# Kernel tuning notes

Measured on AMD Instinct MI355X. Metric: run time of the kernel, lower is better.

The kernel has to match this reference:

```python
import jax, jax.numpy as jnp
import numpy as np

H = 128   # hidden_dim
L = 3     # num_layers
N = 50000
E = 800000
EPS = 1e-5


def setup_inputs() -> dict:
    key = jax.random.key(0)
    ks = jax.random.split(key, 16)
    s = 0.02  # param init scale
    return {
        "edge_index_new": jax.random.randint(ks[0], (2, E), 0, N),
        "aligned_features": jax.random.normal(ks[1], (E, 8), jnp.float32),
        "h_nodes_old": jax.random.normal(ks[2], (N, H), jnp.float32),
        "num_nodes": N,
        # node_fusion: Linear(2H -> H)
        "Wf": jax.random.normal(ks[3], (2 * H, H), jnp.float32) * s,
        "bf": jnp.zeros((H,), jnp.float32),
        # edge_to_weight: Linear(8->H), Linear(H->1)
        "We1": jax.random.normal(ks[4], (8, H), jnp.float32) * s,
        "be1": jnp.zeros((H,), jnp.float32),
        "We2": jax.random.normal(ks[5], (H, 1), jnp.float32) * s,
        "be2": jnp.zeros((1,), jnp.float32),
        # GraphConv per layer: lin_rel (W+b), lin_root (W, no bias)
        "Wrel": jax.random.normal(ks[6], (L, H, H), jnp.float32) * s,
        "brel": jnp.zeros((L, H), jnp.float32),
        "Wroot": jax.random.normal(ks[7], (L, H, H), jnp.float32) * s,
        # LayerNorm per layer
        "gamma": jnp.ones((L, H), jnp.float32),
        "beta": jnp.zeros((L, H), jnp.float32),
        # edge_decoder: Linear(2H+8 -> H), Linear(H -> 1)
        "Wd1": jax.random.normal(ks[8], (2 * H + 8, H), jnp.float32) * s,
        "bd1": jnp.zeros((H,), jnp.float32),
        "Wd2": jax.random.normal(ks[9], (H, 1), jnp.float32) * s,
        "bd2": jnp.zeros((1,), jnp.float32),
    }


def _layer_norm(x, g, b):
    mu = jnp.mean(x, axis=-1, keepdims=True)
    var = jnp.mean((x - mu) ** 2, axis=-1, keepdims=True)
    return (x - mu) * jax.lax.rsqrt(var + EPS) * g + b


def reference(edge_index_new, aligned_features, h_nodes_old, num_nodes,
              Wf, bf, We1, be1, We2, be2,
              Wrel, brel, Wroot, gamma, beta,
              Wd1, bd1, Wd2, bd2):
    dt = h_nodes_old.dtype
    hd = Wf.shape[1]
    # node_fusion(cat([ones, h_old])) ; dropout is identity in eval
    x_init = jnp.ones((num_nodes, hd), dtype=dt)
    x = jax.nn.relu(jnp.concatenate([x_init, h_nodes_old], axis=-1) @ Wf + bf)
    # edge_to_weight -> scalar per edge
    ew = jax.nn.sigmoid(jax.nn.relu(aligned_features @ We1 + be1) @ We2 + be2)[:, 0]
    src, dst = edge_index_new[0], edge_index_new[1]
    n_layers = Wrel.shape[0]
    for l in range(n_layers):
        x_res = x
        # GraphConv: sum_{j->i} w_e * x[j], then lin_rel(agg) + lin_root(x)
        msg = ew[:, None] * x[src]                         # [E, H]
        agg = jax.ops.segment_sum(msg, dst, num_segments=num_nodes)
        h = agg @ Wrel[l] + brel[l] + x @ Wroot[l]
        h = jax.nn.relu(_layer_norm(h, gamma[l], beta[l]))
        x = h + x_res
    # edge decoder on gathered node pairs + raw 8-dim features
    edge_repr = jnp.concatenate([x[src], x[dst], aligned_features], axis=-1)
    hmid = jax.nn.relu(edge_repr @ Wd1 + bd1)
    return hmid @ Wd2 + bd2
```

## Files before the change

### kernel.cpp

```cpp
#include <hip/hip_runtime.h>
#include <hip/hip_bf16.h>

#define H 128
#define LN_EPS 1e-5f

typedef __attribute__((ext_vector_type(8))) short bf16x8;
typedef __attribute__((ext_vector_type(4))) float f32x4;

static __device__ __forceinline__ unsigned short f2bf(float f) {
  unsigned u = __float_as_uint(f);
  unsigned r = (u + 0x7fff + ((u >> 16) & 1)) >> 16;
  return (unsigned short)r;
}
static __device__ __forceinline__ float bf2f(unsigned short s) {
  return __uint_as_float(((unsigned)s) << 16);
}


__global__ void zero_int_kernel(int* __restrict__ p, int n) {
  int i = blockIdx.x * blockDim.x + threadIdx.x;
  if (i < n) p[i] = 0;
}

__global__ __launch_bounds__(1024) void prep_cvec_kernel(const float* __restrict__ Wf,
                                                         const float* __restrict__ bf,
                                                         float* __restrict__ cvec) {
  __shared__ float part[8][128];
  int tid = threadIdx.x;
  int col = tid & 127, seg = tid >> 7;
  float s = 0.f;
  for (int r = seg * 16; r < seg * 16 + 16; ++r) s += Wf[r * H + col];
  part[seg][col] = s;
  __syncthreads();
  if (tid < 128) {
    float t = bf[tid];
#pragma unroll
    for (int g = 0; g < 8; ++g) t += part[g][tid];
    cvec[tid] = t;
  }
}

__global__ void count_kernel(const int* __restrict__ ei, int E, int* __restrict__ cnt) {
  int e = blockIdx.x * blockDim.x + threadIdx.x;
  if (e < E) atomicAdd(&cnt[ei[E + e]], 1);
}

__global__ __launch_bounds__(1024) void scan_kernel(const int* __restrict__ cnt,
                                                    int* __restrict__ off,
                                                    int* __restrict__ pos, int N) {
  __shared__ int wtot[16];
  __shared__ int wbase[16];
  __shared__ int s_btot;
  __shared__ int s_carry;
  int tid = threadIdx.x, lane = tid & 63, wid = tid >> 6;
  if (tid == 0) s_carry = 0;
  __syncthreads();
  for (int base = 0; base < N; base += 4096) {
    int i0 = base + tid * 4;
    int v[4];
#pragma unroll
    for (int j = 0; j < 4; ++j) v[j] = (i0 + j < N) ? cnt[i0 + j] : 0;
    int s = v[0] + v[1] + v[2] + v[3];
    int incl = s;
#pragma unroll
    for (int o = 1; o < 64; o <<= 1) {
      int t = __shfl_up(incl, o, 64);
      if (lane >= o) incl += t;
    }
    if (lane == 63) wtot[wid] = incl;
    __syncthreads();
    if (tid == 0) {
      int run = 0;
      for (int w = 0; w < 16; ++w) { wbase[w] = run; run += wtot[w]; }
      s_btot = run;
    }
    __syncthreads();
    int e0 = s_carry + wbase[wid] + (incl - s);
#pragma unroll
    for (int j = 0; j < 4; ++j) {
      if (i0 + j < N) { off[i0 + j] = e0; pos[i0 + j] = e0; }
      e0 += v[j];
    }
    __syncthreads();
    if (tid == 0) s_carry += s_btot;
    __syncthreads();
  }
  if (tid == 0) off[N] = s_carry;
}

__global__ __launch_bounds__(256) void pack_w_kernel(const float* __restrict__ Wf,
                                                     const float* __restrict__ Wrel,
                                                     const float* __restrict__ Wroot,
                                                     const float* __restrict__ Wd1,
                                                     unsigned short* __restrict__ wpk) {
  int id = blockIdx.x * blockDim.x + threadIdx.x;
  if (id >= 9 * 2048) return;
  int l = id & 63, nf = (id >> 6) & 7, kk = (id >> 9) & 3, m = id >> 11;
  const float* src;
  if (m == 0) src = Wf + H * H;
  else if (m <= 3) src = Wrel + (size_t)(m - 1) * H * H;
  else if (m <= 6) src = Wroot + (size_t)(m - 4) * H * H;
  else src = Wd1 + (size_t)(m - 7) * H * H;
  int col = nf * 16 + (l & 15);
  int kbase = kk * 32 + (l >> 4) * 8;
  unsigned short t[8];
#pragma unroll
  for (int j = 0; j < 8; ++j) t[j] = f2bf(src[(size_t)(kbase + j) * H + col]);
  *(uint4*)&wpk[(size_t)id * 8] = *(uint4*)t;
}

__global__ __launch_bounds__(256) void edge_mlp_fill_kernel(
    const int* __restrict__ ei, const float* __restrict__ af, const float* __restrict__ We1,
    const float* __restrict__ be1, const float* __restrict__ We2, const float* __restrict__ be2,
    int* __restrict__ pos, uint2* __restrict__ csr, int* __restrict__ csr_eid, int E) {
  int lane = threadIdx.x & 63;
  int sub = lane & 15;
  int grp = lane >> 4;
  float w1[8][8], b1[8], w2[8];
#pragma unroll
  for (int i = 0; i < 8; ++i)
#pragma unroll
    for (int c = 0; c < 8; ++c) w1[i][c] = We1[i * H + sub * 8 + c];
#pragma unroll
  for (int c = 0; c < 8; ++c) { b1[c] = be1[sub * 8 + c]; w2[c] = We2[sub * 8 + c]; }
  float b2 = be2[0];
  int gw = (blockIdx.x * blockDim.x + threadIdx.x) >> 6;
  int nw = (gridDim.x * blockDim.x) >> 6;
  int n4 = (E + 3) >> 2;
  for (int e4 = gw; e4 < n4; e4 += nw) {
    int e = e4 * 4 + grp;
    bool valid = e < E;
    int ee = valid ? e : E - 1;
    float4 a0 = *(const float4*)&af[(size_t)ee * 8];
    float4 a1 = *(const float4*)&af[(size_t)ee * 8 + 4];
    float afv[8] = {a0.x, a0.y, a0.z, a0.w, a1.x, a1.y, a1.z, a1.w};
    float t[8];
#pragma unroll
    for (int c = 0; c < 8; ++c) t[c] = b1[c];
#pragma unroll
    for (int i = 0; i < 8; ++i)
#pragma unroll
      for (int c = 0; c < 8; ++c) t[c] += afv[i] * w1[i][c];
    float p = 0.f;
#pragma unroll
    for (int c = 0; c < 8; ++c) p += fmaxf(t[c], 0.f) * w2[c];
    p += __shfl_xor(p, 1, 64);
    p += __shfl_xor(p, 2, 64);
    p += __shfl_xor(p, 4, 64);
    p += __shfl_xor(p, 8, 64);
    if (valid && sub == 0) {
      float w = 1.f / (1.f + expf(-(p + b2)));
      int d = ei[E + e];
      int ppos = atomicAdd(&pos[d], 1);
      csr[ppos] = make_uint2((unsigned)ei[e], __float_as_uint(w));
      csr_eid[ppos] = e;
    }
  }
}

__global__ __launch_bounds__(256) void gemm_init_kernel(
    const float* __restrict__ Xf, const unsigned short* __restrict__ Wp,
    const float* __restrict__ bias, unsigned short* __restrict__ Y, int M) {
  int l = threadIdx.x & 63, w = threadIdx.x >> 6;
  int lr = l & 15, lg = l >> 4;
  int m0 = blockIdx.x * 128 + w * 32;
  f32x4 acc[2][8] = {};
  for (int kk = 0; kk < 4; ++kk) {
    bf16x8 a[2];
#pragma unroll
    for (int mi = 0; mi < 2; ++mi) {
      int row = m0 + mi * 16 + lr;
      if (row >= M) row = M - 1;
      const float* xp = &Xf[(size_t)row * H + kk * 32 + lg * 8];
      float4 u0 = *(const float4*)xp;
      float4 u1 = *(const float4*)(xp + 4);
      unsigned short t[8] = {f2bf(u0.x), f2bf(u0.y), f2bf(u0.z), f2bf(u0.w),
                             f2bf(u1.x), f2bf(u1.y), f2bf(u1.z), f2bf(u1.w)};
      a[mi] = *(const bf16x8*)t;
    }
#pragma unroll
    for (int nf = 0; nf < 8; ++nf) {
      bf16x8 b = *(const bf16x8*)&Wp[(size_t)(kk * 8 + nf) * 512 + l * 8];
#pragma unroll
      for (int mi = 0; mi < 2; ++mi)
        acc[mi][nf] = __builtin_amdgcn_mfma_f32_16x16x32_bf16(a[mi], b, acc[mi][nf], 0, 0, 0);
    }
  }
  float bv[8];
#pragma unroll
  for (int nf = 0; nf < 8; ++nf) bv[nf] = bias[nf * 16 + lr];
#pragma unroll
  for (int mi = 0; mi < 2; ++mi)
#pragma unroll
    for (int r = 0; r < 4; ++r) {
      int row = m0 + mi * 16 + lg * 4 + r;
      if (row < M) {
#pragma unroll
        for (int nf = 0; nf < 8; ++nf)
          Y[(size_t)row * H + nf * 16 + lr] = f2bf(fmaxf(acc[mi][nf][r] + bv[nf], 0.f));
      }
    }
}

__global__ __launch_bounds__(256) void gemm_layer_ln_kernel(
    const unsigned short* __restrict__ Agg, const unsigned short* __restrict__ WpRel,
    unsigned short* __restrict__ Xio, const unsigned short* __restrict__ WpRoot,
    const float* __restrict__ brel, const float* __restrict__ gamma,
    const float* __restrict__ beta, int M) {
  int l = threadIdx.x & 63, w = threadIdx.x >> 6;
  int lr = l & 15, lg = l >> 4;
  int m0 = blockIdx.x * 128 + w * 32;
  f32x4 acc[2][8] = {};
  for (int kk = 0; kk < 8; ++kk) {
    const unsigned short* X = (kk >= 4) ? Xio : Agg;
    const unsigned short* Wp = (kk >= 4) ? WpRoot : WpRel;
    int k4 = kk & 3;
    bf16x8 a[2] = {};
#pragma unroll
    for (int mi = 0; mi < 2; ++mi) {
      int row = m0 + mi * 16 + lr;
      if (row < M) a[mi] = *(const bf16x8*)&X[(size_t)row * H + k4 * 32 + lg * 8];
    }
#pragma unroll
    for (int nf = 0; nf < 8; ++nf) {
      bf16x8 b = *(const bf16x8*)&Wp[(size_t)(k4 * 8 + nf) * 512 + l * 8];
#pragma unroll
      for (int mi = 0; mi < 2; ++mi)
        acc[mi][nf] = __builtin_amdgcn_mfma_f32_16x16x32_bf16(a[mi], b, acc[mi][nf], 0, 0, 0);
    }
  }
  float bv[8], gv[8], bev[8];
#pragma unroll
  for (int nf = 0; nf < 8; ++nf) {
    int col = nf * 16 + lr;
    bv[nf] = brel[col]; gv[nf] = gamma[col]; bev[nf] = beta[col];
  }
#pragma unroll
  for (int mi = 0; mi < 2; ++mi) {
#pragma unroll
    for (int r = 0; r < 4; ++r) {
      int row = m0 + mi * 16 + lg * 4 + r;
      float hv[8], s1 = 0.f;
#pragma unroll
      for (int nf = 0; nf < 8; ++nf) { hv[nf] = acc[mi][nf][r] + bv[nf]; s1 += hv[nf]; }
      s1 += __shfl_xor(s1, 1, 64);
      s1 += __shfl_xor(s1, 2, 64);
      s1 += __shfl_xor(s1, 4, 64);
      s1 += __shfl_xor(s1, 8, 64);
      float mu = s1 * (1.0f / H);
      float s2 = 0.f;
#pragma unroll
      for (int nf = 0; nf < 8; ++nf) { float d = hv[nf] - mu; s2 += d * d; }
      s2 += __shfl_xor(s2, 1, 64);
      s2 += __shfl_xor(s2, 2, 64);
      s2 += __shfl_xor(s2, 4, 64);
      s2 += __shfl_xor(s2, 8, 64);
      float rstd = rsqrtf(s2 * (1.0f / H) + LN_EPS);
      if (row < M) {
#pragma unroll
        for (int nf = 0; nf < 8; ++nf) {
          int col = nf * 16 + lr;
          float v = fmaxf((hv[nf] - mu) * rstd * gv[nf] + bev[nf], 0.f);
          v += bf2f(Xio[(size_t)row * H + col]);
          Xio[(size_t)row * H + col] = f2bf(v);
        }
      }
    }
  }
}

__global__ __launch_bounds__(256) void gemm_dec_kernel(
    const unsigned short* __restrict__ X, const unsigned short* __restrict__ WpA,
    const unsigned short* __restrict__ WpB, const float* __restrict__ bd1,
    unsigned short* __restrict__ Aout, unsigned short* __restrict__ Bout, int M) {
  int l = threadIdx.x & 63, w = threadIdx.x >> 6;
  int lr = l & 15, lg = l >> 4;
  int m0 = blockIdx.x * 128 + w * 32;
  f32x4 accA[2][8] = {};
  f32x4 accB[2][8] = {};
  for (int kk = 0; kk < 4; ++kk) {
    bf16x8 a[2];
#pragma unroll
    for (int mi = 0; mi < 2; ++mi) {
      int row = m0 + mi * 16 + lr;
      if (row >= M) row = M - 1;
      a[mi] = *(const bf16x8*)&X[(size_t)row * H + kk * 32 + lg * 8];
    }
#pragma unroll
    for (int nf = 0; nf < 8; ++nf) {
      bf16x8 bA = *(const bf16x8*)&WpA[(size_t)(kk * 8 + nf) * 512 + l * 8];
      bf16x8 bB = *(const bf16x8*)&WpB[(size_t)(kk * 8 + nf) * 512 + l * 8];
#pragma unroll
      for (int mi = 0; mi < 2; ++mi) {
        accA[mi][nf] = __builtin_amdgcn_mfma_f32_16x16x32_bf16(a[mi], bA, accA[mi][nf], 0, 0, 0);
        accB[mi][nf] = __builtin_amdgcn_mfma_f32_16x16x32_bf16(a[mi], bB, accB[mi][nf], 0, 0, 0);
      }
    }
  }
  float bdv[8];
#pragma unroll
  for (int nf = 0; nf < 8; ++nf) bdv[nf] = bd1[nf * 16 + lr];
#pragma unroll
  for (int mi = 0; mi < 2; ++mi)
#pragma unroll
    for (int r = 0; r < 4; ++r) {
      int row = m0 + mi * 16 + lg * 4 + r;
      if (row < M) {
#pragma unroll
        for (int nf = 0; nf < 8; ++nf) {
          int col = nf * 16 + lr;
          Aout[(size_t)row * H + col] = f2bf(accA[mi][nf][r] + bdv[nf]);
          Bout[(size_t)row * H + col] = f2bf(accB[mi][nf][r]);
        }
      }
    }
}

__global__ __launch_bounds__(256) void gather_agg_v3_kernel(
    const unsigned short* __restrict__ xbf, const int* __restrict__ off,
    const uint2* __restrict__ csr, unsigned short* __restrict__ aggbf, int N) {
  int gw = (blockIdx.x * blockDim.x + threadIdx.x) >> 6;
  int lane = threadIdx.x & 63;
  int half = lane >> 5, li = lane & 31;
  int n = gw * 2 + half;
  if (n < N) {
    int s0 = off[n], s1 = off[n + 1];
    float a0 = 0.f, a1 = 0.f, a2 = 0.f, a3 = 0.f;
    for (int base = s0; base < s1; base += 16) {
      uint2 c[16];
#pragma unroll
      for (int j = 0; j < 16; ++j) {
        int id = base + j;
        c[j] = csr[id < s1 ? id : s1 - 1];
        if (id >= s1) c[j].y = 0;
      }
      uint2 v[16];
#pragma unroll
      for (int j = 0; j < 16; ++j)
        v[j] = *(const uint2*)&xbf[(size_t)c[j].x * H + li * 4];
#pragma unroll
      for (int j = 0; j < 16; ++j) {
        float w = __uint_as_float(c[j].y);
        a0 += w * bf2f((unsigned short)(v[j].x & 0xffffu));
        a1 += w * bf2f((unsigned short)(v[j].x >> 16));
        a2 += w * bf2f((unsigned short)(v[j].y & 0xffffu));
        a3 += w * bf2f((unsigned short)(v[j].y >> 16));
      }
    }
    unsigned o0 = (unsigned)f2bf(a0) | ((unsigned)f2bf(a1) << 16);
    unsigned o1 = (unsigned)f2bf(a2) | ((unsigned)f2bf(a3) << 16);
    *(uint2*)&aggbf[(size_t)n * H + li * 4] = make_uint2(o0, o1);
  }
}

__global__ __launch_bounds__(256) void edge_out_v4b_kernel(
    const int* __restrict__ off, const uint2* __restrict__ csr, const int* __restrict__ csr_eid,
    const float* __restrict__ af, const unsigned short* __restrict__ A,
    const unsigned short* __restrict__ B, const float* __restrict__ Wd1c,
    const float* __restrict__ Wd2, const float* __restrict__ bd2, float* __restrict__ out,
    int N) {
  int lane = threadIdx.x & 63;
  int sub = lane & 15;
  int grp = lane >> 4;
  float wc[8][8], w2[8];
#pragma unroll
  for (int i = 0; i < 8; ++i)
#pragma unroll
    for (int c = 0; c < 8; ++c) wc[i][c] = Wd1c[i * H + sub * 8 + c];
#pragma unroll
  for (int c = 0; c < 8; ++c) w2[c] = Wd2[sub * 8 + c];
  float b2 = bd2[0];
  int gg = ((blockIdx.x * blockDim.x + threadIdx.x) >> 6) * 4 + grp;
  int ng = ((gridDim.x * blockDim.x) >> 6) * 4;
  for (int n = gg; n < N; n += ng) {
    int s0 = off[n], s1 = off[n + 1];
    if (s0 >= s1) continue;
    uint4 vb = *(const uint4*)&B[(size_t)n * H + sub * 8];
    const unsigned* pb = (const unsigned*)&vb;
    float tb[8];
#pragma unroll
    for (int q = 0; q < 4; ++q) {
      tb[q * 2 + 0] = bf2f((unsigned short)(pb[q] & 0xffffu));
      tb[q * 2 + 1] = bf2f((unsigned short)(pb[q] >> 16));
    }
    uint2 c = csr[s0];
    int eid = csr_eid[s0];
    uint4 va = *(const uint4*)&A[(size_t)c.x * H + sub * 8];
    float4 f0 = *(const float4*)&af[(size_t)eid * 8];
    float4 f1 = *(const float4*)&af[(size_t)eid * 8 + 4];
    for (int k = s0; k < s1; ++k) {
      uint4 va_c = va;
      float4 g0 = f0, g1 = f1;
      int eid_c = eid;
      if (k + 1 < s1) {
        c = csr[k + 1];
        eid = csr_eid[k + 1];
        va = *(const uint4*)&A[(size_t)c.x * H + sub * 8];
        f0 = *(const float4*)&af[(size_t)eid * 8];
        f1 = *(const float4*)&af[(size_t)eid * 8 + 4];
      }
      const unsigned* pa = (const unsigned*)&va_c;
      float t[8];
#pragma unroll
      for (int q = 0; q < 4; ++q) {
        t[q * 2 + 0] = tb[q * 2 + 0] + bf2f((unsigned short)(pa[q] & 0xffffu));
        t[q * 2 + 1] = tb[q * 2 + 1] + bf2f((unsigned short)(pa[q] >> 16));
      }
      float afv[8] = {g0.x, g0.y, g0.z, g0.w, g1.x, g1.y, g1.z, g1.w};
#pragma unroll
      for (int i = 0; i < 8; ++i)
#pragma unroll
        for (int cc = 0; cc < 8; ++cc) t[cc] += afv[i] * wc[i][cc];
      float p = 0.f;
#pragma unroll
      for (int cc = 0; cc < 8; ++cc) p += fmaxf(t[cc], 0.f) * w2[cc];
      p += __shfl_xor(p, 1, 64);
      p += __shfl_xor(p, 2, 64);
      p += __shfl_xor(p, 4, 64);
      p += __shfl_xor(p, 8, 64);
      if (sub == 0) out[eid_c] = p + b2;
    }
  }
}

extern "C" void kernel_launch(void* const* d_in, const int* in_sizes, int n_in, void* d_out,
                              int out_size, void* d_ws, size_t ws_size, hipStream_t stream) {
  const int* ei = (const int*)d_in[0];
  const float* af = (const float*)d_in[1];
  const float* h_old = (const float*)d_in[2];
  const float* Wf = (const float*)d_in[4];
  const float* bf = (const float*)d_in[5];
  const float* We1 = (const float*)d_in[6];
  const float* be1 = (const float*)d_in[7];
  const float* We2 = (const float*)d_in[8];
  const float* be2 = (const float*)d_in[9];
  const float* Wrel = (const float*)d_in[10];
  const float* brel = (const float*)d_in[11];
  const float* Wroot = (const float*)d_in[12];
  const float* gamma = (const float*)d_in[13];
  const float* beta = (const float*)d_in[14];
  const float* Wd1 = (const float*)d_in[15];
  const float* bd1 = (const float*)d_in[16];
  const float* Wd2 = (const float*)d_in[17];
  const float* bd2 = (const float*)d_in[18];
  const int N = in_sizes[2] / H;
  const int E = in_sizes[1] / 8;
  float* out = (float*)d_out;

  char* p = (char*)d_ws;
  auto alloc = [&](size_t b) { char* r = p; p += (b + 255) & ~(size_t)255; return r; };
  int* cnt = (int*)alloc((size_t)N * 4);
  int* pos = (int*)alloc((size_t)N * 4);
  int* off = (int*)alloc((size_t)(N + 1) * 4);
  uint2* csr = (uint2*)alloc((size_t)E * 8);
  int* csr_eid = (int*)alloc((size_t)E * 4);
  float* cvec = (float*)alloc(H * 4);
  unsigned short* wpk = (unsigned short*)alloc((size_t)9 * 16384 * 2);
  unsigned short* xbf = (unsigned short*)alloc((size_t)N * H * 2);
  unsigned short* aggbf = (unsigned short*)alloc((size_t)N * H * 2);
  unsigned short* buf2 = (unsigned short*)alloc((size_t)N * H * 2);

  unsigned short* Abf = aggbf;
  unsigned short* Bbf = buf2;

  hipLaunchKernelGGL(zero_int_kernel, dim3((N + 255) / 256), dim3(256), 0, stream, cnt, N);
  hipLaunchKernelGGL(prep_cvec_kernel, dim3(1), dim3(1024), 0, stream, Wf, bf, cvec);
  hipLaunchKernelGGL(count_kernel, dim3((E + 255) / 256), dim3(256), 0, stream, ei, E, cnt);
  hipLaunchKernelGGL(scan_kernel, dim3(1), dim3(1024), 0, stream, cnt, off, pos, N);
  hipLaunchKernelGGL(edge_mlp_fill_kernel, dim3(4096), dim3(256), 0, stream, ei, af, We1, be1,
                     We2, be2, pos, csr, csr_eid, E);
  hipLaunchKernelGGL(pack_w_kernel, dim3(72), dim3(256), 0, stream, Wf, Wrel, Wroot, Wd1, wpk);

  int gblocks = (N + 127) / 128;
  hipLaunchKernelGGL(gemm_init_kernel, dim3(gblocks), dim3(256), 0, stream, h_old, wpk, cvec,
                     xbf, N);

  int gat_blocks = (N / 2 + 3) / 4;
  for (int l = 0; l < 3; ++l) {
    hipLaunchKernelGGL(gather_agg_v3_kernel, dim3(gat_blocks), dim3(256), 0, stream, xbf, off,
                       csr, aggbf, N);
    hipLaunchKernelGGL(gemm_layer_ln_kernel, dim3(gblocks), dim3(256), 0, stream, aggbf,
                       wpk + (size_t)(1 + l) * 16384, xbf, wpk + (size_t)(4 + l) * 16384,
                       brel + l * H, gamma + l * H, beta + l * H, N);
  }

  hipLaunchKernelGGL(gemm_dec_kernel, dim3(gblocks), dim3(256), 0, stream, xbf,
                     wpk + (size_t)7 * 16384, wpk + (size_t)8 * 16384, bd1, Abf, Bbf, N);
  hipLaunchKernelGGL(edge_out_v4b_kernel, dim3((N + 15) / 16), dim3(256), 0, stream, off, csr,
                     csr_eid, af, Abf, Bbf, Wd1 + 2 * H * H, Wd2, bd2, out, N);
}
```

Before: 473.3 us.

## Split edge weight MLP from CSR fill and pack CSR entries as uint4

Edge weights are now computed in a separate kernel into a temporary array. A dedicated per-edge kernel then scatters src, weight and edge id into a single 16-byte CSR record using atomics. This replaces the fused kernel that did the atomics from only one lane per 16, and it lets the decoder load one record instead of two separate arrays. In exchange there is an extra launch, an extra E-sized array, and wider CSR records that the gather kernel reads at 16-byte stride while using only 8 bytes.

```diff
diff --git a/kernel.cpp b/kernel.cpp
--- a/kernel.cpp
+++ b/kernel.cpp
@@ -109,10 +109,9 @@
   *(uint4*)&wpk[(size_t)id * 8] = *(uint4*)t;
 }
 
-__global__ __launch_bounds__(256) void edge_mlp_fill_kernel(
-    const int* __restrict__ ei, const float* __restrict__ af, const float* __restrict__ We1,
-    const float* __restrict__ be1, const float* __restrict__ We2, const float* __restrict__ be2,
-    int* __restrict__ pos, uint2* __restrict__ csr, int* __restrict__ csr_eid, int E) {
+__global__ __launch_bounds__(256) void edge_weight_v3_kernel(
+    const float* __restrict__ af, const float* __restrict__ We1, const float* __restrict__ be1,
+    const float* __restrict__ We2, const float* __restrict__ be2, float* __restrict__ ew, int E) {
   int lane = threadIdx.x & 63;
   int sub = lane & 15;
   int grp = lane >> 4;
@@ -149,12 +148,19 @@
     p += __shfl_xor(p, 4, 64);
     p += __shfl_xor(p, 8, 64);
     if (valid && sub == 0) {
-      float w = 1.f / (1.f + expf(-(p + b2)));
-      int d = ei[E + e];
-      int ppos = atomicAdd(&pos[d], 1);
-      csr[ppos] = make_uint2((unsigned)ei[e], __float_as_uint(w));
-      csr_eid[ppos] = e;
-    }
+      float s = p + b2;
+      ew[e] = 1.f / (1.f + expf(-s));
+    }
+  }
+}
+
+__global__ void fill_v2_kernel(const int* __restrict__ ei, const float* __restrict__ ew, int E,
+                               int* __restrict__ pos, uint4* __restrict__ csr4) {
+  int e = blockIdx.x * blockDim.x + threadIdx.x;
+  if (e < E) {
+    int d = ei[E + e];
+    int p = atomicAdd(&pos[d], 1);
+    csr4[p] = make_uint4((unsigned)ei[e], __float_as_uint(ew[e]), (unsigned)e, 0u);
   }
 }
 
@@ -318,7 +324,7 @@
 
 __global__ __launch_bounds__(256) void gather_agg_v3_kernel(
     const unsigned short* __restrict__ xbf, const int* __restrict__ off,
-    const uint2* __restrict__ csr, unsigned short* __restrict__ aggbf, int N) {
+    const uint4* __restrict__ csr4, unsigned short* __restrict__ aggbf, int N) {
   int gw = (blockIdx.x * blockDim.x + threadIdx.x) >> 6;
   int lane = threadIdx.x & 63;
   int half = lane >> 5, li = lane & 31;
@@ -331,7 +337,7 @@
 #pragma unroll
       for (int j = 0; j < 16; ++j) {
         int id = base + j;
-        c[j] = csr[id < s1 ? id : s1 - 1];
+        c[j] = *(const uint2*)&csr4[id < s1 ? id : s1 - 1];
         if (id >= s1) c[j].y = 0;
       }
       uint2 v[16];
@@ -353,12 +359,11 @@
   }
 }
 
-__global__ __launch_bounds__(256) void edge_out_v4b_kernel(
-    const int* __restrict__ off, const uint2* __restrict__ csr, const int* __restrict__ csr_eid,
-    const float* __restrict__ af, const unsigned short* __restrict__ A,
-    const unsigned short* __restrict__ B, const float* __restrict__ Wd1c,
-    const float* __restrict__ Wd2, const float* __restrict__ bd2, float* __restrict__ out,
-    int N) {
+__global__ __launch_bounds__(256) void edge_out_v4c_kernel(
+    const int* __restrict__ off, const uint4* __restrict__ csr4, const float* __restrict__ af,
+    const unsigned short* __restrict__ A, const unsigned short* __restrict__ B,
+    const float* __restrict__ Wd1c, const float* __restrict__ Wd2,
+    const float* __restrict__ bd2, float* __restrict__ out, int N) {
   int lane = threadIdx.x & 63;
   int sub = lane & 15;
   int grp = lane >> 4;
@@ -383,21 +388,21 @@
       tb[q * 2 + 0] = bf2f((unsigned short)(pb[q] & 0xffffu));
       tb[q * 2 + 1] = bf2f((unsigned short)(pb[q] >> 16));
     }
-    uint2 c = csr[s0];
-    int eid = csr_eid[s0];
+    uint4 c = csr4[s0];
     uint4 va = *(const uint4*)&A[(size_t)c.x * H + sub * 8];
-    float4 f0 = *(const float4*)&af[(size_t)eid * 8];
-    float4 f1 = *(const float4*)&af[(size_t)eid * 8 + 4];
+    float4 f0 = *(const float4*)&af[(size_t)c.z * 8];
+    float4 f1 = *(const float4*)&af[(size_t)c.z * 8 + 4];
+    int eid = (int)c.z;
     for (int k = s0; k < s1; ++k) {
       uint4 va_c = va;
       float4 g0 = f0, g1 = f1;
       int eid_c = eid;
       if (k + 1 < s1) {
-        c = csr[k + 1];
-        eid = csr_eid[k + 1];
+        c = csr4[k + 1];
+        eid = (int)c.z;
         va = *(const uint4*)&A[(size_t)c.x * H + sub * 8];
-        f0 = *(const float4*)&af[(size_t)eid * 8];
-        f1 = *(const float4*)&af[(size_t)eid * 8 + 4];
+        f0 = *(const float4*)&af[(size_t)c.z * 8];
+        f1 = *(const float4*)&af[(size_t)c.z * 8 + 4];
       }
       const unsigned* pa = (const unsigned*)&va_c;
       float t[8];
@@ -452,8 +457,8 @@
   int* cnt = (int*)alloc((size_t)N * 4);
   int* pos = (int*)alloc((size_t)N * 4);
   int* off = (int*)alloc((size_t)(N + 1) * 4);
-  uint2* csr = (uint2*)alloc((size_t)E * 8);
-  int* csr_eid = (int*)alloc((size_t)E * 4);
+  uint4* csr4 = (uint4*)alloc((size_t)E * 16);
+  float* ew = (float*)alloc((size_t)E * 4);
   float* cvec = (float*)alloc(H * 4);
   unsigned short* wpk = (unsigned short*)alloc((size_t)9 * 16384 * 2);
   unsigned short* xbf = (unsigned short*)alloc((size_t)N * H * 2);
@@ -467,8 +472,10 @@
   hipLaunchKernelGGL(prep_cvec_kernel, dim3(1), dim3(1024), 0, stream, Wf, bf, cvec);
   hipLaunchKernelGGL(count_kernel, dim3((E + 255) / 256), dim3(256), 0, stream, ei, E, cnt);
   hipLaunchKernelGGL(scan_kernel, dim3(1), dim3(1024), 0, stream, cnt, off, pos, N);
-  hipLaunchKernelGGL(edge_mlp_fill_kernel, dim3(4096), dim3(256), 0, stream, ei, af, We1, be1,
-                     We2, be2, pos, csr, csr_eid, E);
+  hipLaunchKernelGGL(edge_weight_v3_kernel, dim3(4096), dim3(256), 0, stream, af, We1, be1,
+                     We2, be2, ew, E);
+  hipLaunchKernelGGL(fill_v2_kernel, dim3((E + 255) / 256), dim3(256), 0, stream, ei, ew, E,
+                     pos, csr4);
   hipLaunchKernelGGL(pack_w_kernel, dim3(72), dim3(256), 0, stream, Wf, Wrel, Wroot, Wd1, wpk);
 
   int gblocks = (N + 127) / 128;
@@ -478,7 +485,7 @@
   int gat_blocks = (N / 2 + 3) / 4;
   for (int l = 0; l < 3; ++l) {
     hipLaunchKernelGGL(gather_agg_v3_kernel, dim3(gat_blocks), dim3(256), 0, stream, xbf, off,
-                       csr, aggbf, N);
+                       csr4, aggbf, N);
     hipLaunchKernelGGL(gemm_layer_ln_kernel, dim3(gblocks), dim3(256), 0, stream, aggbf,
                        wpk + (size_t)(1 + l) * 16384, xbf, wpk + (size_t)(4 + l) * 16384,
                        brel + l * H, gamma + l * H, beta + l * H, N);
@@ -486,6 +493,6 @@
 
   hipLaunchKernelGGL(gemm_dec_kernel, dim3(gblocks), dim3(256), 0, stream, xbf,
                      wpk + (size_t)7 * 16384, wpk + (size_t)8 * 16384, bd1, Abf, Bbf, N);
-  hipLaunchKernelGGL(edge_out_v4b_kernel, dim3((N + 15) / 16), dim3(256), 0, stream, off, csr,
-                     csr_eid, af, Abf, Bbf, Wd1 + 2 * H * H, Wd2, bd2, out, N);
-}
+  hipLaunchKernelGGL(edge_out_v4c_kernel, dim3((N + 15) / 16), dim3(256), 0, stream, off, csr4,
+                     af, Abf, Bbf, Wd1 + 2 * H * H, Wd2, bd2, out, N);
+}
```

Result: slower. 497.4 us (+5.1%).
